# Optimization experiments

Hardware: AMD Instinct MI355X
Metric: run time of the kernel (lower is better)

Reference implementation:

```python
import jax, jax.numpy as jnp
import numpy as np


def _cdist_p2(x, y):
    # x: [N, t1, h], y: [N, t2, h] -> [N, t1, t2] Euclidean distances
    x2 = jnp.sum(x * x, axis=-1)  # [N, t1]
    y2 = jnp.sum(y * y, axis=-1)  # [N, t2]
    xy = jnp.einsum('nik,njk->nij', x, y)  # [N, t1, t2]
    d2 = x2[:, :, None] + y2[None if False else slice(None), None, :] - 2.0 * xy
    d2 = jnp.maximum(d2, 0.0)
    return jnp.sqrt(d2)


def _solve_relaxed_wmd(scores, axis):
    # argmin + one-hot scatter + (mask*scores).mean() == sum of per-slice minima / scores.size
    idx = jnp.argmin(scores, axis=axis, keepdims=True)
    mins = jnp.take_along_axis(scores, idx, axis=axis)
    return jnp.sum(mins) / scores.size


def setup_inputs() -> dict:
    key = jax.random.key(0)
    kx, ky = jax.random.split(key)
    L, B, t1, t2, h = 4, 16, 1024, 1024, 128
    x = jax.random.normal(kx, (L, B, t1, h), dtype=jnp.float32)
    y = jax.random.normal(ky, (L, B, t2, h), dtype=jnp.float32)
    return {"x": x, "y": y}


def reference(x, y):
    L, B, t1, h = x.shape
    t2 = y.shape[2]
    xf = x.reshape(L * B, t1, h).astype(jnp.float32)
    yf = y.reshape(L * B, t2, h).astype(jnp.float32)
    scores = _cdist_p2(xf, yf)  # [L*B, t1, t2]
    forward_scores = _solve_relaxed_wmd(scores, axis=1)
    backward_scores = _solve_relaxed_wmd(scores, axis=2)
    return jnp.maximum(forward_scores, backward_scores)
```

## Files before the change

### kernel.cpp

```cpp
#include <hip/hip_runtime.h>

#define NB 64
#define T 1024
#define HD 128

#define EINF 0xFF800000u

typedef __attribute__((ext_vector_type(8))) short bf16x8;
typedef __attribute__((ext_vector_type(4))) float f32x4;

static __device__ __forceinline__ short f2bf(float f) {
    unsigned u = __float_as_uint(f);
    u += 0x7FFFu + ((u >> 16) & 1u);
    return (short)(u >> 16);
}
static __device__ __forceinline__ unsigned fenc(float f) {
    unsigned b = __float_as_uint(f);
    return b ^ (unsigned)(((int)b >> 31) | (int)0x80000000);
}
static __device__ __forceinline__ float fdec(unsigned u) {
    unsigned m = (~(unsigned)((int)u >> 31)) | 0x80000000u;
    return __uint_as_float(u ^ m);
}

__global__ void wmd_prep(const float* __restrict__ y, short* __restrict__ ybf,
                         float* __restrict__ y2,
                         unsigned* __restrict__ g_colmin, unsigned* __restrict__ g_rowmin,
                         float* __restrict__ sums, unsigned* __restrict__ batch_cnt,
                         unsigned* __restrict__ g_cnt) {
    int gi = blockIdx.x * 256 + threadIdx.x;
    float4 vy = reinterpret_cast<const float4*>(y)[gi];
    short4 sy;
    sy.x = f2bf(vy.x); sy.y = f2bf(vy.y); sy.z = f2bf(vy.z); sy.w = f2bf(vy.w);
    reinterpret_cast<short4*>(ybf)[gi] = sy;
    float py = vy.x * vy.x + vy.y * vy.y + vy.z * vy.z + vy.w * vy.w;
    py += __shfl_xor(py, 1);  py += __shfl_xor(py, 2);  py += __shfl_xor(py, 4);
    py += __shfl_xor(py, 8);  py += __shfl_xor(py, 16);
    if ((threadIdx.x & 31) == 0) y2[gi >> 5] = py;
    if (gi < NB * T) { g_colmin[gi] = EINF; g_rowmin[gi] = EINF; }
    if (gi < 2) sums[gi] = 0.f;
    if (gi >= 4 && gi < 4 + NB) batch_cnt[gi - 4] = 0u;
    if (gi == 4 + NB) g_cnt[0] = 0u;
}

__global__ __launch_bounds__(256, 4)
void wmd_main(const float* __restrict__ x, const short* __restrict__ ybf,
              const float* __restrict__ y2g,
              unsigned* __restrict__ g_colmin, unsigned* __restrict__ g_rowmin,
              float* __restrict__ sums, unsigned* __restrict__ batch_cnt,
              unsigned* __restrict__ g_cnt, float* __restrict__ out) {
    __shared__ short b_sm[2][64 * 128];
    __shared__ float y2_sm[512];
    __shared__ float x2_sm[128];
    __shared__ unsigned col_min_sm[512];
    __shared__ unsigned last_sm;
    __shared__ float red_sm[8];

    const int tid  = threadIdx.x;
    const int lin  = blockIdx.y * 16 + blockIdx.x;
    const int m    = (lin >> 3) & 7;
    const int grp  = ((lin >> 6) << 3) | (lin & 7);
    const int n    = grp >> 1;
    const int i0   = m * 128;
    const int j0   = (grp & 1) * 512;
    const int lane = tid & 63;
    const int wave = tid >> 6;
    const int l16  = lane & 15, quad = lane >> 4;
    const float FINF = __uint_as_float(0x7F800000u);

    #pragma unroll
    for (int e = tid; e < 512; e += 256) col_min_sm[e] = EINF;

#define ISSUE_GLLS(pbuf, jtile)                                                   \
    {                                                                             \
        const short* ybase = ybf + (((size_t)(n * T + j0 + (jtile) * 64)) << 7);  \
        _Pragma("unroll")                                                         \
        for (int it = 0; it < 4; ++it) {                                          \
            int g   = wave * 4 + it;                                              \
            int s   = g * 64 + lane;                                              \
            int row = s >> 4;                                                     \
            int c   = (s & 15) ^ (row & 7);                                       \
            const short* gp = ybase + row * 128 + c * 8;                          \
            __builtin_amdgcn_global_load_lds(                                     \
                (const __attribute__((address_space(1))) void*)gp,                \
                (__attribute__((address_space(3))) void*)&b_sm[pbuf][g * 512],    \
                16, 0, 0);                                                        \
        }                                                                         \
    }

    ISSUE_GLLS(0, 0);

    bf16x8 af[2][4];
    #pragma unroll
    for (int mi = 0; mi < 2; ++mi) {
        float part = 0.f;
        #pragma unroll
        for (int kk = 0; kk < 4; ++kk) {
            const float4* gp = reinterpret_cast<const float4*>(
                x + (((size_t)(n * T + i0 + wave * 32 + mi * 16 + l16)) << 7) + kk * 32 + quad * 8);
            float4 a = gp[0], b = gp[1];
            bf16x8 f;
            f[0] = f2bf(a.x); f[1] = f2bf(a.y); f[2] = f2bf(a.z); f[3] = f2bf(a.w);
            f[4] = f2bf(b.x); f[5] = f2bf(b.y); f[6] = f2bf(b.z); f[7] = f2bf(b.w);
            af[mi][kk] = f;
            part += a.x * a.x + a.y * a.y + a.z * a.z + a.w * a.w;
            part += b.x * b.x + b.y * b.y + b.z * b.z + b.w * b.w;
        }
        part += __shfl_xor(part, 16);
        part += __shfl_xor(part, 32);
        if (quad == 0) x2_sm[wave * 32 + mi * 16 + l16] = part;
    }
    #pragma unroll
    for (int e = tid; e < 512; e += 256) y2_sm[e] = y2g[n * T + j0 + e];

    float rmin[8];
    #pragma unroll
    for (int q = 0; q < 8; ++q) rmin[q] = FINF;

    __syncthreads();

    float x2v[8];
    #pragma unroll
    for (int mi = 0; mi < 2; ++mi)
        #pragma unroll
        for (int r = 0; r < 4; ++r)
            x2v[mi * 4 + r] = x2_sm[wave * 32 + mi * 16 + quad * 4 + r];

    for (int jt = 0; jt < 8; ++jt) {
        const int p = jt & 1;
        if (jt < 7) ISSUE_GLLS(p ^ 1, jt + 1);

        float y2v[4];
        #pragma unroll
        for (int ni = 0; ni < 4; ++ni)
            y2v[ni] = y2_sm[jt * 64 + ni * 16 + l16];

        f32x4 acc[2][4];
        #pragma unroll
        for (int mi = 0; mi < 2; ++mi)
            #pragma unroll
            for (int ni = 0; ni < 4; ++ni) {
                f32x4 z = {0.f, 0.f, 0.f, 0.f};
                acc[mi][ni] = z;
            }

        #pragma unroll
        for (int kk = 0; kk < 4; ++kk) {
            bf16x8 bv[4];
            #pragma unroll
            for (int ni = 0; ni < 4; ++ni) {
                int row = ni * 16 + l16;
                int c   = (kk * 4 + quad) ^ (row & 7);
                bv[ni] = *reinterpret_cast<const bf16x8*>(&b_sm[p][(row * 16 + c) * 8]);
            }
            #pragma unroll
            for (int mi = 0; mi < 2; ++mi)
                #pragma unroll
                for (int ni = 0; ni < 4; ++ni)
                    acc[mi][ni] = __builtin_amdgcn_mfma_f32_16x16x32_bf16(
                        af[mi][kk], bv[ni], acc[mi][ni], 0, 0, 0);
        }

        float vcol[4] = {FINF, FINF, FINF, FINF};
        #pragma unroll
        for (int mi = 0; mi < 2; ++mi)
            #pragma unroll
            for (int r = 0; r < 4; ++r) {
                float x2r = x2v[mi * 4 + r];
                #pragma unroll
                for (int ni = 0; ni < 4; ++ni) {
                    float xy = acc[mi][ni][r];
                    rmin[mi * 4 + r] = fminf(rmin[mi * 4 + r], fmaf(-2.f, xy, y2v[ni]));
                    vcol[ni]         = fminf(vcol[ni],         fmaf(-2.f, xy, x2r));
                }
            }
        #pragma unroll
        for (int ni = 0; ni < 4; ++ni) {
            float v = vcol[ni];
            v = fminf(v, __shfl_xor(v, 16));
            v = fminf(v, __shfl_xor(v, 32));
            if (lane < 16)
                atomicMin(&col_min_sm[jt * 64 + ni * 16 + lane], fenc(v));
        }
        __syncthreads();
    }

    #pragma unroll
    for (int e = tid; e < 512; e += 256) {
        float v = fdec(col_min_sm[e]) + y2_sm[e];
        atomicMin(&g_colmin[n * T + j0 + e], fenc(v));
    }
    #pragma unroll
    for (int mi = 0; mi < 2; ++mi)
        #pragma unroll
        for (int r = 0; r < 4; ++r) {
            float v = rmin[mi * 4 + r] + x2v[mi * 4 + r];
            v = fminf(v, __shfl_xor(v, 1));
            v = fminf(v, __shfl_xor(v, 2));
            v = fminf(v, __shfl_xor(v, 4));
            v = fminf(v, __shfl_xor(v, 8));
            if (l16 == 0)
                atomicMin(&g_rowmin[n * T + i0 + wave * 32 + mi * 16 + quad * 4 + r], fenc(v));
        }

    __builtin_amdgcn_s_waitcnt(0);
    __syncthreads();
    if (tid == 0)
        last_sm = __hip_atomic_fetch_add(&batch_cnt[n], 1u, __ATOMIC_RELAXED,
                                         __HIP_MEMORY_SCOPE_AGENT);
    __syncthreads();
    if (last_sm != 15u) return;

    float sc = 0.f, sr = 0.f;
    for (int e = tid; e < T; e += 256) {
        unsigned cu = __hip_atomic_load(&g_colmin[n * T + e], __ATOMIC_RELAXED,
                                        __HIP_MEMORY_SCOPE_AGENT);
        unsigned ru = __hip_atomic_load(&g_rowmin[n * T + e], __ATOMIC_RELAXED,
                                        __HIP_MEMORY_SCOPE_AGENT);
        sc += sqrtf(fmaxf(fdec(cu), 0.f));
        sr += sqrtf(fmaxf(fdec(ru), 0.f));
    }
    #pragma unroll
    for (int o = 1; o < 64; o <<= 1) {
        sc += __shfl_xor(sc, o);
        sr += __shfl_xor(sr, o);
    }
    if (lane == 0) { red_sm[wave] = sc; red_sm[4 + wave] = sr; }
    __syncthreads();
    if (tid == 0) {
        atomicAdd(&sums[0], red_sm[0] + red_sm[1] + red_sm[2] + red_sm[3]);
        atomicAdd(&sums[1], red_sm[4] + red_sm[5] + red_sm[6] + red_sm[7]);
        __builtin_amdgcn_s_waitcnt(0);
        unsigned old = __hip_atomic_fetch_add(g_cnt, 1u, __ATOMIC_RELAXED,
                                              __HIP_MEMORY_SCOPE_AGENT);
        if (old == NB - 1) {
            float a = __hip_atomic_load(&sums[0], __ATOMIC_RELAXED, __HIP_MEMORY_SCOPE_AGENT);
            float b = __hip_atomic_load(&sums[1], __ATOMIC_RELAXED, __HIP_MEMORY_SCOPE_AGENT);
            out[0] = fmaxf(a, b) * (1.0f / 67108864.0f);
        }
    }
}

extern "C" void kernel_launch(void* const* d_in, const int* in_sizes, int n_in,
                              void* d_out, int out_size, void* d_ws, size_t ws_size,
                              hipStream_t stream) {
    const float* x = (const float*)d_in[0];
    const float* y = (const float*)d_in[1];
    float* out = (float*)d_out;

    char* ws = (char*)d_ws;
    unsigned* g_colmin  = (unsigned*)(ws);
    unsigned* g_rowmin  = (unsigned*)(ws + 256 * 1024);
    float*    y2g       = (float*)(ws + 512 * 1024);
    float*    sums      = (float*)(ws + 768 * 1024);
    unsigned* batch_cnt = (unsigned*)(ws + 768 * 1024 + 256);
    unsigned* g_cnt     = (unsigned*)(ws + 768 * 1024 + 2048);
    short*    ybf       = (short*)(ws + 1024 * 1024);

    wmd_prep<<<(NB * T * HD / 4) / 256, 256, 0, stream>>>(
        y, ybf, y2g, g_colmin, g_rowmin, sums, batch_cnt, g_cnt);
    wmd_main<<<dim3(16, NB), 256, 0, stream>>>(
        x, ybf, y2g, g_colmin, g_rowmin, sums, batch_cnt, g_cnt, out);
}
```

Before: 126.8 us.

## Split j-range into quarters, drop LDS side buffers, use shuffles and global atomics

Doubles the grid so each block covers 256 columns instead of 512, doubling the number of blocks per batch. It removes the shared-memory y2, x2, column-min and reduction buffers, using register shuffles for x2/y2 and atomicMin straight to global column minima each tile, and reuses the B tile buffer for the tail reduction. The launch bound goes to 5 blocks per CU to raise occupancy. In exchange, A-fragment loads and x2 computation are repeated across twice as many blocks, and global atomic traffic for column minima grows.

Result: slower. 355.3 us (+180.1%).

```diff
diff --git a/kernel.cpp b/kernel.cpp
--- a/kernel.cpp
+++ b/kernel.cpp
@@ -43,33 +43,25 @@
     if (gi == 4 + NB) g_cnt[0] = 0u;
 }
 
-__global__ __launch_bounds__(256, 4)
+__global__ __launch_bounds__(256, 5)
 void wmd_main(const float* __restrict__ x, const short* __restrict__ ybf,
               const float* __restrict__ y2g,
               unsigned* __restrict__ g_colmin, unsigned* __restrict__ g_rowmin,
               float* __restrict__ sums, unsigned* __restrict__ batch_cnt,
               unsigned* __restrict__ g_cnt, float* __restrict__ out) {
     __shared__ short b_sm[2][64 * 128];
-    __shared__ float y2_sm[512];
-    __shared__ float x2_sm[128];
-    __shared__ unsigned col_min_sm[512];
-    __shared__ unsigned last_sm;
-    __shared__ float red_sm[8];
 
     const int tid  = threadIdx.x;
-    const int lin  = blockIdx.y * 16 + blockIdx.x;
+    const int lin  = blockIdx.y * 32 + blockIdx.x;
     const int m    = (lin >> 3) & 7;
     const int grp  = ((lin >> 6) << 3) | (lin & 7);
-    const int n    = grp >> 1;
+    const int n    = grp >> 2;
     const int i0   = m * 128;
-    const int j0   = (grp & 1) * 512;
+    const int j0   = (grp & 3) * 256;
     const int lane = tid & 63;
     const int wave = tid >> 6;
     const int l16  = lane & 15, quad = lane >> 4;
     const float FINF = __uint_as_float(0x7F800000u);
-
-    #pragma unroll
-    for (int e = tid; e < 512; e += 256) col_min_sm[e] = EINF;
 
 #define ISSUE_GLLS(pbuf, jtile)                                                   \
     {                                                                             \
@@ -91,9 +83,10 @@
     ISSUE_GLLS(0, 0);
 
     bf16x8 af[2][4];
+    float part[2];
     #pragma unroll
     for (int mi = 0; mi < 2; ++mi) {
-        float part = 0.f;
+        float p = 0.f;
         #pragma unroll
         for (int kk = 0; kk < 4; ++kk) {
             const float4* gp = reinterpret_cast<const float4*>(
@@ -103,15 +96,24 @@
             f[0] = f2bf(a.x); f[1] = f2bf(a.y); f[2] = f2bf(a.z); f[3] = f2bf(a.w);
             f[4] = f2bf(b.x); f[5] = f2bf(b.y); f[6] = f2bf(b.z); f[7] = f2bf(b.w);
             af[mi][kk] = f;
-            part += a.x * a.x + a.y * a.y + a.z * a.z + a.w * a.w;
-            part += b.x * b.x + b.y * b.y + b.z * b.z + b.w * b.w;
-        }
-        part += __shfl_xor(part, 16);
-        part += __shfl_xor(part, 32);
-        if (quad == 0) x2_sm[wave * 32 + mi * 16 + l16] = part;
-    }
-    #pragma unroll
-    for (int e = tid; e < 512; e += 256) y2_sm[e] = y2g[n * T + j0 + e];
+            p += a.x * a.x + a.y * a.y + a.z * a.z + a.w * a.w;
+            p += b.x * b.x + b.y * b.y + b.z * b.z + b.w * b.w;
+        }
+        p += __shfl_xor(p, 16);
+        p += __shfl_xor(p, 32);
+        part[mi] = p;
+    }
+    float x2v[8];
+    #pragma unroll
+    for (int mi = 0; mi < 2; ++mi)
+        #pragma unroll
+        for (int r = 0; r < 4; ++r)
+            x2v[mi * 4 + r] = __shfl(part[mi], quad * 4 + r);
+
+    float y2r[4];
+    #pragma unroll
+    for (int q = 0; q < 4; ++q)
+        y2r[q] = y2g[n * T + j0 + q * 64 + lane];
 
     float rmin[8];
     #pragma unroll
@@ -119,21 +121,14 @@
 
     __syncthreads();
 
-    float x2v[8];
-    #pragma unroll
-    for (int mi = 0; mi < 2; ++mi)
-        #pragma unroll
-        for (int r = 0; r < 4; ++r)
-            x2v[mi * 4 + r] = x2_sm[wave * 32 + mi * 16 + quad * 4 + r];
-
-    for (int jt = 0; jt < 8; ++jt) {
+    for (int jt = 0; jt < 4; ++jt) {
         const int p = jt & 1;
-        if (jt < 7) ISSUE_GLLS(p ^ 1, jt + 1);
+        if (jt < 3) ISSUE_GLLS(p ^ 1, jt + 1);
 
         float y2v[4];
         #pragma unroll
         for (int ni = 0; ni < 4; ++ni)
-            y2v[ni] = y2_sm[jt * 64 + ni * 16 + l16];
+            y2v[ni] = __shfl(y2r[jt], ni * 16 + l16);
 
         f32x4 acc[2][4];
         #pragma unroll
@@ -179,17 +174,13 @@
             float v = vcol[ni];
             v = fminf(v, __shfl_xor(v, 16));
             v = fminf(v, __shfl_xor(v, 32));
+            v += y2v[ni];
             if (lane < 16)
-                atomicMin(&col_min_sm[jt * 64 + ni * 16 + lane], fenc(v));
+                atomicMin(&g_colmin[n * T + j0 + jt * 64 + ni * 16 + lane], fenc(v));
         }
         __syncthreads();
     }
 
-    #pragma unroll
-    for (int e = tid; e < 512; e += 256) {
-        float v = fdec(col_min_sm[e]) + y2_sm[e];
-        atomicMin(&g_colmin[n * T + j0 + e], fenc(v));
-    }
     #pragma unroll
     for (int mi = 0; mi < 2; ++mi)
         #pragma unroll
@@ -203,13 +194,15 @@
                 atomicMin(&g_rowmin[n * T + i0 + wave * 32 + mi * 16 + quad * 4 + r], fenc(v));
         }
 
+    unsigned* tail_u = (unsigned*)&b_sm[0][0];
+    float*    tail_f = (float*)&b_sm[0][0];
     __builtin_amdgcn_s_waitcnt(0);
     __syncthreads();
     if (tid == 0)
-        last_sm = __hip_atomic_fetch_add(&batch_cnt[n], 1u, __ATOMIC_RELAXED,
-                                         __HIP_MEMORY_SCOPE_AGENT);
-    __syncthreads();
-    if (last_sm != 15u) return;
+        tail_u[0] = __hip_atomic_fetch_add(&batch_cnt[n], 1u, __ATOMIC_RELAXED,
+                                           __HIP_MEMORY_SCOPE_AGENT);
+    __syncthreads();
+    if (tail_u[0] != 31u) return;
 
     float sc = 0.f, sr = 0.f;
     for (int e = tid; e < T; e += 256) {
@@ -225,11 +218,12 @@
         sc += __shfl_xor(sc, o);
         sr += __shfl_xor(sr, o);
     }
-    if (lane == 0) { red_sm[wave] = sc; red_sm[4 + wave] = sr; }
+    __syncthreads();
+    if (lane == 0) { tail_f[1 + wave] = sc; tail_f[5 + wave] = sr; }
     __syncthreads();
     if (tid == 0) {
-        atomicAdd(&sums[0], red_sm[0] + red_sm[1] + red_sm[2] + red_sm[3]);
-        atomicAdd(&sums[1], red_sm[4] + red_sm[5] + red_sm[6] + red_sm[7]);
+        atomicAdd(&sums[0], tail_f[1] + tail_f[2] + tail_f[3] + tail_f[4]);
+        atomicAdd(&sums[1], tail_f[5] + tail_f[6] + tail_f[7] + tail_f[8]);
         __builtin_amdgcn_s_waitcnt(0);
         unsigned old = __hip_atomic_fetch_add(g_cnt, 1u, __ATOMIC_RELAXED,
                                               __HIP_MEMORY_SCOPE_AGENT);
@@ -259,6 +253,6 @@
 
     wmd_prep<<<(NB * T * HD / 4) / 256, 256, 0, stream>>>(
         y, ybf, y2g, g_colmin, g_rowmin, sums, batch_cnt, g_cnt);
-    wmd_main<<<dim3(16, NB), 256, 0, stream>>>(
+    wmd_main<<<dim3(32, NB), 256, 0, stream>>>(
         x, ybf, y2g, g_colmin, g_rowmin, sums, batch_cnt, g_cnt, out);
 }
```
